# Kernel optimization log

Measured on AMD Instinct MI355X. Metric: run time of the kernel, lower is better.

Reference implementation:

```python
import jax, jax.numpy as jnp
import numpy as np

B, N, Q, Z, C, L = 1, 6, 20000, 4, 128, 4
IMG_H, IMG_W = 256, 704
PC_RANGE = (-50.0, -50.0, -4.0, 50.0, 50.0, 4.0)
NUM_FREQS = 10
EPS = 1e-5
LEVEL_HW = ((64, 176), (32, 88), (16, 44), (8, 22))


def _mlp(x, ws, bs):
    for i, (w, b) in enumerate(zip(ws, bs)):
        x = x @ w + b
        if i < len(ws) - 1:
            x = jax.nn.relu(x)
    return x


def _bilinear(feat_hwc, px, py):
    # feat_hwc: [H, W, C]; px, py: [P] pixel coords. align_corners=False, zero padding.
    H, W, _ = feat_hwc.shape
    x0 = jnp.floor(px).astype(jnp.int32)
    y0 = jnp.floor(py).astype(jnp.int32)
    wx = px - x0
    wy = py - y0

    def gather(yi, xi):
        inb = ((yi >= 0) & (yi < H) & (xi >= 0) & (xi < W)).astype(feat_hwc.dtype)
        return feat_hwc[jnp.clip(yi, 0, H - 1), jnp.clip(xi, 0, W - 1)] * inb[:, None]

    return (gather(y0, x0) * ((1 - wy) * (1 - wx))[:, None]
          + gather(y0, x0 + 1) * ((1 - wy) * wx)[:, None]
          + gather(y0 + 1, x0) * (wy * (1 - wx))[:, None]
          + gather(y0 + 1, x0 + 1) * (wy * wx)[:, None])


def _pointbev_forward(feats, reference_points, lidar2img,
                      pe_w1, pe_b1, pe_w2, pe_b2, wt_w, wt_b, hm_ws, hm_bs):
    pos = jnp.transpose(reference_points, (0, 2, 1, 3))            # [B,Q,Z,3] in [0,1]
    # sinusoidal positional encoding map (normalized=False: coords used as-is)
    freqs = (2.0 ** jnp.arange(NUM_FREQS, dtype=pos.dtype)) * jnp.pi
    ang = pos[..., None] * freqs                                   # [B,Q,Z,3,F]
    pe_in = jnp.concatenate([jnp.sin(ang), jnp.cos(ang)], axis=-1)
    pe_in = pe_in.reshape(pos.shape[:-1] + (3 * 2 * NUM_FREQS,))
    pos_emb = _mlp(pe_in, [pe_w1, pe_w2], [pe_b1, pe_b2])          # [B,Q,Z,C]
    scale_w = jax.nn.softmax(pos_emb @ wt_w + wt_b, axis=-1)       # [B,Q,Z,L]

    # unnormalize to metric lidar coords via pc_range
    lo = jnp.asarray(PC_RANGE[:3], pos.dtype)
    span = jnp.asarray(PC_RANGE[3:], pos.dtype) - lo
    pts4 = jnp.concatenate([pos * span + lo, jnp.ones_like(pos[..., :1])], axis=-1)
    cam = jnp.einsum('bnij,bqzj->bnqzi', lidar2img, pts4)          # [B,N,Q,Z,4]
    homo = cam[..., 2]
    uv = cam[..., :2] / jnp.maximum(homo, EPS)[..., None]
    u = uv[..., 0] / IMG_W
    v = uv[..., 1] / IMG_H
    valid = ((homo > EPS) & (u > 0.0) & (u < 1.0) & (v > 0.0) & (v < 1.0)).astype(pos.dtype)

    sampler = jax.vmap(_bilinear)
    uf = u.reshape(B * N, Q * Z)
    vf = v.reshape(B * N, Q * Z)
    out = jnp.zeros((B, Q, Z, C), pos.dtype)
    for l, feat in enumerate(feats):                               # L=4 fixed levels
        Hl, Wl = feat.shape[2], feat.shape[3]
        s = sampler(feat.reshape(B * N, Hl, Wl, C), uf * Wl - 0.5, vf * Hl - 0.5)
        s = s.reshape(B, N, Q, Z, C) * valid[..., None]            # mask invalid projections
        out = out + s.sum(axis=1) * scale_w[..., l, None]          # sum views, weight level
    out = (out + pos_emb).reshape(B, Q, Z * C)
    return _mlp(out, hm_ws, hm_bs)                                 # [B,Q,C]


def setup_inputs():
    key = jax.random.key(0)
    ks = jax.random.split(key, 32)
    inp = {}
    for l, (h, w) in enumerate(LEVEL_HW):
        inp[f"feat{l}"] = jax.random.normal(ks[l], (B, N, h, w, C), jnp.float32)
    inp["reference_points"] = jax.random.uniform(ks[8], (B, Z, Q, 3), jnp.float32)
    # structured nuScenes-like lidar2img = intrinsics @ extrinsics for a 6-camera ring
    l2i = np.zeros((B, N, 4, 4), np.float32)
    K = np.array([[400.0, 0.0, IMG_W / 2, 0.0],
                  [0.0, 400.0, IMG_H / 2, 0.0],
                  [0.0, 0.0, 1.0, 0.0],
                  [0.0, 0.0, 0.0, 1.0]], np.float32)
    for n in range(N):
        yaw = 2.0 * np.pi * n / N
        cy, sy = np.cos(yaw), np.sin(yaw)
        R = np.array([[-sy, cy, 0.0], [0.0, 0.0, -1.0], [cy, sy, 0.0]], np.float32)
        E = np.eye(4, dtype=np.float32)
        E[:3, :3] = R
        E[:3, 3] = [0.0, 1.5, 0.5]
        l2i[0, n] = K @ E
    inp["lidar2img"] = jnp.asarray(l2i)

    def lin(k, fi, fo):
        s = 1.0 / np.sqrt(fi)
        return jax.random.uniform(k, (fi, fo), jnp.float32, -s, s)

    d_in = 3 * 2 * NUM_FREQS
    inp["pe_w1"] = lin(ks[9], d_in, 2 * C); inp["pe_b1"] = jnp.zeros((2 * C,), jnp.float32)
    inp["pe_w2"] = lin(ks[10], 2 * C, C);   inp["pe_b2"] = jnp.zeros((C,), jnp.float32)
    inp["wt_w"] = lin(ks[11], C, L);        inp["wt_b"] = jnp.zeros((L,), jnp.float32)
    dims = [Z * C, 2 * Z * C, 2 * Z * C, 2 * Z * C, C]
    for i in range(4):
        inp[f"hm_w{i+1}"] = lin(ks[12 + i], dims[i], dims[i + 1])
        inp[f"hm_b{i+1}"] = jnp.zeros((dims[i + 1],), jnp.float32)
    return inp


def reference(feat0, feat1, feat2, feat3, reference_points, lidar2img,
              pe_w1, pe_b1, pe_w2, pe_b2, wt_w, wt_b,
              hm_w1, hm_b1, hm_w2, hm_b2, hm_w3, hm_b3, hm_w4, hm_b4):
    return _pointbev_forward((feat0, feat1, feat2, feat3), reference_points, lidar2img,
                             pe_w1, pe_b1, pe_w2, pe_b2, wt_w, wt_b,
                             [hm_w1, hm_w2, hm_w3, hm_w4], [hm_b1, hm_b2, hm_b3, hm_b4])
```

## Files before the change

### kernel.cpp

```cpp
#include <hip/hip_runtime.h>
#include <math.h>

#define QN 20000
#define PN 80000
#define CN 128
#define NVIEW 6

typedef __attribute__((ext_vector_type(8))) _Float16 h8;
typedef __attribute__((ext_vector_type(4))) _Float16 h4;
typedef __attribute__((ext_vector_type(4))) float f32x4;

__device__ __forceinline__ void gload16(const void* g, void* l) {
  __builtin_amdgcn_global_load_lds(
      (const __attribute__((address_space(1))) void*)g,
      (__attribute__((address_space(3))) void*)l, 16, 0, 0);
}

__global__ __launch_bounds__(256) void wtrans_all(
    const float* __restrict__ w0, const float* __restrict__ w1,
    const float* __restrict__ w2, const float* __restrict__ w3,
    const float* __restrict__ w4, const float* __restrict__ w5,
    _Float16* __restrict__ base) {
  __shared__ float t[32][33];
  int b = blockIdx.x;
  const float* W; _Float16* T; int K, N, Kp, nbx, lb;
  if (b < 16)        { W = w0; T = base + 0;       K = 60;   N = 256;  Kp = 64;   nbx = 8;  lb = b; }
  else if (b < 48)   { W = w1; T = base + 32768;   K = 256;  N = 128;  Kp = 256;  nbx = 4;  lb = b - 16; }
  else if (b < 560)  { W = w2; T = base + 98304;   K = 512;  N = 1024; Kp = 512;  nbx = 32; lb = b - 48; }
  else if (b < 1584) { W = w3; T = base + 1146880; K = 1024; N = 1024; Kp = 1024; nbx = 32; lb = b - 560; }
  else if (b < 2608) { W = w4; T = base + 3244032; K = 1024; N = 1024; Kp = 1024; nbx = 32; lb = b - 1584; }
  else               { W = w5; T = base + 5341184; K = 1024; N = 128;  Kp = 1024; nbx = 4;  lb = b - 2608; }
  const int n0 = (lb % nbx) * 32, k0 = (lb / nbx) * 32;
  const int tx = threadIdx.x & 31, ty = threadIdx.x >> 5;
  #pragma unroll
  for (int j = 0; j < 4; ++j) {
    int k = k0 + ty + j * 8;
    t[ty + j * 8][tx] = (k < K) ? W[(size_t)k * N + n0 + tx] : 0.f;
  }
  __syncthreads();
  #pragma unroll
  for (int j = 0; j < 4; ++j) {
    int n = n0 + ty + j * 8;
    int k = k0 + tx;
    T[(size_t)n * Kp + k] = (_Float16)t[tx][ty + j * 8];
  }
}

__global__ __launch_bounds__(256) void fcvt_kernel(
    const float* __restrict__ s0, const float* __restrict__ s1,
    const float* __restrict__ s2, const float* __restrict__ s3,
    _Float16* __restrict__ d) {
  size_t i = (size_t)blockIdx.x * 256 + threadIdx.x;
  if (i >= 2872320) return;
  const float* s; size_t off;
  if (i < 2162688)      { s = s0; off = 0; }
  else if (i < 2703360) { s = s1; off = 2162688; }
  else if (i < 2838528) { s = s2; off = 2703360; }
  else                  { s = s3; off = 2838528; }
  f32x4 v = *(const f32x4*)(s + (i - off) * 4);
  h4 o;
  o[0] = (_Float16)v[0]; o[1] = (_Float16)v[1];
  o[2] = (_Float16)v[2]; o[3] = (_Float16)v[3];
  *(h4*)(d + i * 4) = o;
}

__global__ __launch_bounds__(256) void pe_in_kernel(const float* __restrict__ rp,
                                                    _Float16* __restrict__ P) {
  int idx = blockIdx.x * 256 + threadIdx.x;
  if (idx >= PN * 64) return;
  int p = idx >> 6, k = idx & 63;
  float val = 0.f;
  if (k < 60) {
    int q = p >> 2, z = p & 3;
    int d = k / 20, r = k - d * 20;
    int j = (r >= 10) ? (r - 10) : r;
    float pos = rp[((size_t)z * QN + q) * 3 + d];
    float ang = pos * ((float)(1 << j) * 3.14159265358979323846f);
    val = (r >= 10) ? cosf(ang) : sinf(ang);
  }
  P[idx] = (_Float16)val;
}

template <bool RELU, int OUT>
__global__ __launch_bounds__(256, 4) void gemm_h(const _Float16* __restrict__ A,
                                                 const _Float16* __restrict__ B,
                                                 const float* __restrict__ bias,
                                                 float* __restrict__ Cf,
                                                 _Float16* __restrict__ Ch,
                                                 int M, int N, int K,
                                                 int nbn) {
  __shared__ _Float16 sm[2][2][4096];
  const int tid = threadIdx.x;
  const int wave = tid >> 6, lane = tid & 63;
  const int wr = wave >> 1, wc = wave & 1;
  const int g = lane >> 4, r16 = lane & 15;

  const int nwg = gridDim.x;
  const int q8 = nwg >> 3, r8 = nwg & 7;
  const int xcd = blockIdx.x & 7, sub = blockIdx.x >> 3;
  const int wg = (xcd < r8 ? xcd * (q8 + 1) : r8 * (q8 + 1) + (xcd - r8) * q8) + sub;
  const int bn = (wg % nbn) * 128;
  const int bm = (wg / nbn) * 128;
  const int nt = K >> 5;

  f32x4 acc[4][4];
  #pragma unroll
  for (int i = 0; i < 4; ++i)
    #pragma unroll
    for (int j = 0; j < 4; ++j) acc[i][j] = {0.f, 0.f, 0.f, 0.f};

  auto STAGE = [&](int buf, int t) {
    const int kof = t << 5;
    const int rsub = lane >> 2;
    const int slot0 = lane & 3;
    #pragma unroll
    for (int pl = 0; pl < 2; ++pl) {
      const _Float16* P = (pl == 0) ? A : B;
      const int rbase = (pl == 0) ? bm : bn;
      #pragma unroll
      for (int i = 0; i < 2; ++i) {
        int group = wave * 2 + i;
        int row = group * 16 + rsub;
        int slot = slot0 ^ ((row >> 1) & 3);
        int gr = rbase + row;
        if (pl == 0 && gr >= M) gr = M - 1;
        gload16(P + (size_t)gr * K + kof + slot * 8,
                &sm[buf][pl][group * 512]);
      }
    }
  };

  auto COMPUTE = [&](int buf) {
    h8 a[4], b[4];
    #pragma unroll
    for (int mi = 0; mi < 4; ++mi) {
      int row = wr * 64 + mi * 16 + r16;
      int off = row * 32 + ((g ^ ((row >> 1) & 3)) * 8);
      a[mi] = *(const h8*)&sm[buf][0][off];
    }
    #pragma unroll
    for (int ni = 0; ni < 4; ++ni) {
      int row = wc * 64 + ni * 16 + r16;
      int off = row * 32 + ((g ^ ((row >> 1) & 3)) * 8);
      b[ni] = *(const h8*)&sm[buf][1][off];
    }
    #pragma unroll
    for (int mi = 0; mi < 4; ++mi)
      #pragma unroll
      for (int ni = 0; ni < 4; ++ni)
        acc[mi][ni] = __builtin_amdgcn_mfma_f32_16x16x32_f16(a[mi], b[ni], acc[mi][ni], 0, 0, 0);
  };

  STAGE(0, 0);
  __syncthreads();

  for (int t = 0; t < nt; ++t) {
    if (t + 1 < nt) STAGE((t + 1) & 1, t + 1);
    COMPUTE(t & 1);
    __syncthreads();
  }

  #pragma unroll
  for (int mi = 0; mi < 4; ++mi) {
    int gr0 = bm + wr * 64 + mi * 16 + (lane >> 4) * 4;
    #pragma unroll
    for (int ni = 0; ni < 4; ++ni) {
      int gc = bn + wc * 64 + ni * 16 + r16;
      float bv = bias[gc];
      #pragma unroll
      for (int r = 0; r < 4; ++r) {
        int row = gr0 + r;
        if (row >= M) continue;
        float v = acc[mi][ni][r] + bv;
        if (RELU) v = fmaxf(v, 0.f);
        if (OUT == 0) Cf[(size_t)row * N + gc] = v;
        else          Ch[(size_t)row * N + gc] = (_Float16)v;
      }
    }
  }
}

__global__ __launch_bounds__(256) void sample_kernel(
    const _Float16* __restrict__ fbase,
    const float* __restrict__ rp, const float* __restrict__ l2i,
    const float* __restrict__ wtw, const float* __restrict__ wtb,
    const _Float16* __restrict__ posE, _Float16* __restrict__ X0) {
  __shared__ float sl2i[96];
  __shared__ float swtT[512];
  __shared__ float sb[4];
  const int tid = threadIdx.x;
  if (tid < 96) sl2i[tid] = l2i[tid];
  for (int i = tid; i < 512; i += 256) swtT[(i & 3) * 128 + (i >> 2)] = wtw[i];
  if (tid < 4) sb[tid] = wtb[tid];
  __syncthreads();

  const _Float16* FL[4] = {fbase, fbase + 8650752, fbase + 10813440,
                           fbase + 11354112};

  const int wave = tid >> 6, lane = tid & 63;
  const int half = lane >> 5, s = lane & 31;
  const int p = blockIdx.x * 8 + wave * 2 + half;
  const int q = p >> 2, z = p & 3;

  const float X  = rp[((size_t)z * QN + q) * 3 + 0] * 100.f - 50.f;
  const float Y  = rp[((size_t)z * QN + q) * 3 + 1] * 100.f - 50.f;
  const float Zc = rp[((size_t)z * QN + q) * 3 + 2] * 8.f - 4.f;

  const int c0 = s * 4;
  h4 pa = *(const h4*)(posE + (size_t)p * CN + c0);
  const float pe0 = (float)pa[0], pe1 = (float)pa[1];
  const float pe2 = (float)pa[2], pe3 = (float)pa[3];

  float l0 = pe0 * swtT[0 * 128 + c0] + pe1 * swtT[0 * 128 + c0 + 1]
           + pe2 * swtT[0 * 128 + c0 + 2] + pe3 * swtT[0 * 128 + c0 + 3];
  float l1 = pe0 * swtT[1 * 128 + c0] + pe1 * swtT[1 * 128 + c0 + 1]
           + pe2 * swtT[1 * 128 + c0 + 2] + pe3 * swtT[1 * 128 + c0 + 3];
  float l2 = pe0 * swtT[2 * 128 + c0] + pe1 * swtT[2 * 128 + c0 + 1]
           + pe2 * swtT[2 * 128 + c0 + 2] + pe3 * swtT[2 * 128 + c0 + 3];
  float l3 = pe0 * swtT[3 * 128 + c0] + pe1 * swtT[3 * 128 + c0 + 1]
           + pe2 * swtT[3 * 128 + c0 + 2] + pe3 * swtT[3 * 128 + c0 + 3];
  #pragma unroll
  for (int off = 16; off > 0; off >>= 1) {
    l0 += __shfl_xor(l0, off);
    l1 += __shfl_xor(l1, off);
    l2 += __shfl_xor(l2, off);
    l3 += __shfl_xor(l3, off);
  }
  l0 += sb[0]; l1 += sb[1]; l2 += sb[2]; l3 += sb[3];
  float mx = fmaxf(fmaxf(l0, l1), fmaxf(l2, l3));
  float ex0 = __expf(l0 - mx), ex1 = __expf(l1 - mx);
  float ex2 = __expf(l2 - mx), ex3 = __expf(l3 - mx);
  float esr = 1.f / (ex0 + ex1 + ex2 + ex3);
  float swl[4] = {ex0 * esr, ex1 * esr, ex2 * esr, ex3 * esr};

  float a0 = 0.f, a1 = 0.f, a2 = 0.f, a3 = 0.f;
  for (int n = 0; n < NVIEW; n++) {
    const float* Mx = sl2i + n * 16;
    float cam0 = Mx[0] * X + Mx[1] * Y + Mx[2]  * Zc + Mx[3];
    float cam1 = Mx[4] * X + Mx[5] * Y + Mx[6]  * Zc + Mx[7];
    float cam2 = Mx[8] * X + Mx[9] * Y + Mx[10] * Zc + Mx[11];
    float denom = fmaxf(cam2, 1e-5f);
    float u = cam0 / denom * (1.f / 704.f);
    float v = cam1 / denom * (1.f / 256.f);
    bool valid = (cam2 > 1e-5f) & (u > 0.f) & (u < 1.f) & (v > 0.f) & (v < 1.f);
    if (!valid) continue;
    float px3 = u * 22.f - 0.5f, py3 = v * 8.f - 0.5f;
    bool interior = (px3 >= 0.f) & (py3 >= 0.f) & (px3 < 21.f) & (py3 < 7.f);
    if (interior) {
      #pragma unroll
      for (int l = 0; l < 4; l++) {
        const int Hl = 64 >> l, Wl = 176 >> l;
        float pxl = u * (float)Wl - 0.5f;
        float pyl = v * (float)Hl - 0.5f;
        float fx = floorf(pxl), fy = floorf(pyl);
        int x0 = (int)fx, y0 = (int)fy;
        float wx = pxl - fx, wy = pyl - fy;
        float w1r = wy * swl[l], w0r = swl[l] - w1r;
        float w01 = w0r * wx, w00 = w0r - w01;
        float w11 = w1r * wx, w10 = w1r - w11;
        const _Float16* cp = FL[l]
            + ((size_t)n * (Hl * Wl) + (size_t)(y0 * Wl + x0)) * CN + c0;
        h4 v00 = *(const h4*)(cp);
        h4 v01 = *(const h4*)(cp + CN);
        h4 v10 = *(const h4*)(cp + Wl * CN);
        h4 v11 = *(const h4*)(cp + Wl * CN + CN);
        a0 = fmaf(w00, (float)v00[0], fmaf(w01, (float)v01[0], fmaf(w10, (float)v10[0], fmaf(w11, (float)v11[0], a0))));
        a1 = fmaf(w00, (float)v00[1], fmaf(w01, (float)v01[1], fmaf(w10, (float)v10[1], fmaf(w11, (float)v11[1], a1))));
        a2 = fmaf(w00, (float)v00[2], fmaf(w01, (float)v01[2], fmaf(w10, (float)v10[2], fmaf(w11, (float)v11[2], a2))));
        a3 = fmaf(w00, (float)v00[3], fmaf(w01, (float)v01[3], fmaf(w10, (float)v10[3], fmaf(w11, (float)v11[3], a3))));
      }
    } else {
      #pragma unroll
      for (int l = 0; l < 4; l++) {
        const int Hl = 64 >> l, Wl = 176 >> l;
        float pxl = u * (float)Wl - 0.5f;
        float pyl = v * (float)Hl - 0.5f;
        float fx = floorf(pxl), fy = floorf(pyl);
        int x0 = (int)fx, y0 = (int)fy;
        float wx = pxl - fx, wy = pyl - fy;
        float w1r = wy * swl[l], w0r = swl[l] - w1r;
        const float wxs[2] = {1.f - wx, wx};
        const float wrs[2] = {w0r, w1r};
        const _Float16* fb = FL[l] + (size_t)n * (Hl * Wl) * CN;
        #pragma unroll
        for (int cy = 0; cy < 2; cy++) {
          #pragma unroll
          for (int cx = 0; cx < 2; cx++) {
            int xi = x0 + cx, yi = y0 + cy;
            bool inb = ((unsigned)xi < (unsigned)Wl) & ((unsigned)yi < (unsigned)Hl);
            int off = inb ? (yi * Wl + xi) * CN : 0;
            float wgt = inb ? (wrs[cy] * wxs[cx]) : 0.f;
            h4 vv = *(const h4*)(fb + off + c0);
            a0 = fmaf(wgt, (float)vv[0], a0);
            a1 = fmaf(wgt, (float)vv[1], a1);
            a2 = fmaf(wgt, (float)vv[2], a2);
            a3 = fmaf(wgt, (float)vv[3], a3);
          }
        }
      }
    }
  }
  h4 o;
  o[0] = (_Float16)(a0 + pe0);
  o[1] = (_Float16)(a1 + pe1);
  o[2] = (_Float16)(a2 + pe2);
  o[3] = (_Float16)(a3 + pe3);
  *(h4*)&X0[(size_t)p * CN + c0] = o;
}

extern "C" void kernel_launch(void* const* d_in, const int* in_sizes, int n_in,
                              void* d_out, int out_size, void* d_ws, size_t ws_size,
                              hipStream_t stream) {
  const float* feat0 = (const float*)d_in[0];
  const float* feat1 = (const float*)d_in[1];
  const float* feat2 = (const float*)d_in[2];
  const float* feat3 = (const float*)d_in[3];
  const float* rp    = (const float*)d_in[4];
  const float* l2i   = (const float*)d_in[5];
  const float* pe_w1 = (const float*)d_in[6];
  const float* pe_b1 = (const float*)d_in[7];
  const float* pe_w2 = (const float*)d_in[8];
  const float* pe_b2 = (const float*)d_in[9];
  const float* wt_w  = (const float*)d_in[10];
  const float* wt_b  = (const float*)d_in[11];
  const float* hm_w1 = (const float*)d_in[12];
  const float* hm_b1 = (const float*)d_in[13];
  const float* hm_w2 = (const float*)d_in[14];
  const float* hm_b2 = (const float*)d_in[15];
  const float* hm_w3 = (const float*)d_in[16];
  const float* hm_b3 = (const float*)d_in[17];
  const float* hm_w4 = (const float*)d_in[18];
  const float* hm_b4 = (const float*)d_in[19];
  float* out = (float*)d_out;

  char* ws = (char*)d_ws;
  typedef _Float16 h16;
  h16* wPE1 = (h16*)(ws + 0);
  h16* wPE2 = (h16*)(ws + 65536);
  h16* wH1  = (h16*)(ws + 196608);
  h16* wH2  = (h16*)(ws + 2293760);
  h16* wH3  = (h16*)(ws + 6488064);
  h16* wH4  = (h16*)(ws + 10682368);

  h16* posE = (h16*)(ws + 11534336);
  h16* hpe  = (h16*)(ws + 53000192);
  h16* pein = (h16*)(ws + 94000128);
  h16* X0   = (h16*)(ws + 53000192);
  h16* H1   = (h16*)(ws + 94000128);
  h16* H2   = (h16*)(ws + 11534336);
  h16* H3   = (h16*)(ws + 94000128);
  h16* f16b = (h16*)(ws + 136000000);

  wtrans_all<<<2736, 256, 0, stream>>>(pe_w1, pe_w2, hm_w1, hm_w2, hm_w3, hm_w4,
                                       (h16*)ws);
  fcvt_kernel<<<(2872320 + 255) / 256, 256, 0, stream>>>(feat0, feat1, feat2,
                                                         feat3, f16b);

  pe_in_kernel<<<(PN * 64 + 255) / 256, 256, 0, stream>>>(rp, pein);

  gemm_h<true, 1><<<2 * 625, 256, 0, stream>>>(pein, wPE1, pe_b1, nullptr, hpe, PN, 256, 64, 2);
  gemm_h<false, 1><<<1 * 625, 256, 0, stream>>>(hpe, wPE2, pe_b2, nullptr, posE, PN, 128, 256, 1);

  sample_kernel<<<PN / 8, 256, 0, stream>>>(f16b, rp, l2i, wt_w, wt_b, posE, X0);

  gemm_h<true, 1><<<8 * 157, 256, 0, stream>>>(X0, wH1, hm_b1, nullptr, H1, QN, 1024, 512, 8);
  gemm_h<true, 1><<<8 * 157, 256, 0, stream>>>(H1, wH2, hm_b2, nullptr, H2, QN, 1024, 1024, 8);
  gemm_h<true, 1><<<8 * 157, 256, 0, stream>>>(H2, wH3, hm_b3, nullptr, H3, QN, 1024, 1024, 8);
  gemm_h<false, 0><<<1 * 157, 256, 0, stream>>>(H3, wH4, hm_b4, out, nullptr, QN, 128, 1024, 1);
}
```

Baseline: 320.2 us.

## Use smaller-tile GEMM for narrow layers and split softmax weights into own kernel

Adds a 64x128-tile GEMM variant with 128-thread blocks and uses it for the two N=128 layers (PE second layer and final head layer). This doubles the workgroup count so more CUs are busy. Separately, the scale-weight softmax moves out of sample_kernel into a dedicated lw_kernel that writes four floats per point to workspace. That trims per-thread work and shared memory in the gather kernel, at the cost of an extra launch and extra global traffic.

```diff
diff --git a/kernel.cpp b/kernel.cpp
--- a/kernel.cpp
+++ b/kernel.cpp
@@ -81,6 +81,50 @@
   P[idx] = (_Float16)val;
 }
 
+__global__ __launch_bounds__(256) void lw_kernel(const _Float16* __restrict__ posE,
+                                                 const float* __restrict__ wtw,
+                                                 const float* __restrict__ wtb,
+                                                 float* __restrict__ lw) {
+  __shared__ float swtT[512];
+  __shared__ float sb[4];
+  const int tid = threadIdx.x;
+  for (int i = tid; i < 512; i += 256) swtT[(i & 3) * 128 + (i >> 2)] = wtw[i];
+  if (tid < 4) sb[tid] = wtb[tid];
+  __syncthreads();
+
+  const int wave = tid >> 6, lane = tid & 63;
+  const int grp = lane >> 4, s = lane & 15;
+  const int p = blockIdx.x * 16 + wave * 4 + grp;
+  const int c0 = s * 8;
+  h8 pa = *(const h8*)(posE + (size_t)p * CN + c0);
+
+  float lg[4];
+  #pragma unroll
+  for (int l = 0; l < 4; ++l) {
+    const float* w = swtT + l * 128 + c0;
+    float acc = 0.f;
+    #pragma unroll
+    for (int j = 0; j < 8; ++j) acc = fmaf((float)pa[j], w[j], acc);
+    lg[l] = acc;
+  }
+  #pragma unroll
+  for (int off = 8; off > 0; off >>= 1) {
+    lg[0] += __shfl_xor(lg[0], off);
+    lg[1] += __shfl_xor(lg[1], off);
+    lg[2] += __shfl_xor(lg[2], off);
+    lg[3] += __shfl_xor(lg[3], off);
+  }
+  lg[0] += sb[0]; lg[1] += sb[1]; lg[2] += sb[2]; lg[3] += sb[3];
+  float mx = fmaxf(fmaxf(lg[0], lg[1]), fmaxf(lg[2], lg[3]));
+  float e0 = __expf(lg[0] - mx), e1 = __expf(lg[1] - mx);
+  float e2 = __expf(lg[2] - mx), e3 = __expf(lg[3] - mx);
+  float esr = 1.f / (e0 + e1 + e2 + e3);
+  if (s == 0) {
+    f32x4 o = {e0 * esr, e1 * esr, e2 * esr, e3 * esr};
+    *(f32x4*)(lw + (size_t)p * 4) = o;
+  }
+}
+
 template <bool RELU, int OUT>
 __global__ __launch_bounds__(256, 4) void gemm_h(const _Float16* __restrict__ A,
                                                  const _Float16* __restrict__ B,
@@ -180,18 +224,114 @@
   }
 }
 
+template <bool RELU, int OUT>
+__global__ __launch_bounds__(128, 3) void gemm_h64(const _Float16* __restrict__ A,
+                                                   const _Float16* __restrict__ B,
+                                                   const float* __restrict__ bias,
+                                                   float* __restrict__ Cf,
+                                                   _Float16* __restrict__ Ch,
+                                                   int M, int N, int K,
+                                                   int nbn) {
+  __shared__ _Float16 smA[2][64 * 32];
+  __shared__ _Float16 smB[2][128 * 32];
+  const int tid = threadIdx.x;
+  const int wave = tid >> 6, lane = tid & 63;
+  const int wc = wave;
+  const int g = lane >> 4, r16 = lane & 15;
+
+  const int nwg = gridDim.x;
+  const int q8 = nwg >> 3, r8 = nwg & 7;
+  const int xcd = blockIdx.x & 7, sub = blockIdx.x >> 3;
+  const int wg = (xcd < r8 ? xcd * (q8 + 1) : r8 * (q8 + 1) + (xcd - r8) * q8) + sub;
+  const int bn = (wg % nbn) * 128;
+  const int bm = (wg / nbn) * 64;
+  const int nt = K >> 5;
+
+  f32x4 acc[4][4];
+  #pragma unroll
+  for (int i = 0; i < 4; ++i)
+    #pragma unroll
+    for (int j = 0; j < 4; ++j) acc[i][j] = {0.f, 0.f, 0.f, 0.f};
+
+  auto STAGE = [&](int buf, int t) {
+    const int kof = t << 5;
+    const int rsub = lane >> 2;
+    const int slot0 = lane & 3;
+    #pragma unroll
+    for (int i = 0; i < 2; ++i) {
+      int group = wave * 2 + i;
+      int row = group * 16 + rsub;
+      int slot = slot0 ^ ((row >> 1) & 3);
+      int gr = bm + row; if (gr >= M) gr = M - 1;
+      gload16(A + (size_t)gr * K + kof + slot * 8, &smA[buf][group * 512]);
+    }
+    #pragma unroll
+    for (int i = 0; i < 4; ++i) {
+      int group = wave * 4 + i;
+      int row = group * 16 + rsub;
+      int slot = slot0 ^ ((row >> 1) & 3);
+      gload16(B + (size_t)(bn + row) * K + kof + slot * 8, &smB[buf][group * 512]);
+    }
+  };
+
+  auto COMPUTE = [&](int buf) {
+    h8 a[4], b[4];
+    #pragma unroll
+    for (int mi = 0; mi < 4; ++mi) {
+      int row = mi * 16 + r16;
+      int off = row * 32 + ((g ^ ((row >> 1) & 3)) * 8);
+      a[mi] = *(const h8*)&smA[buf][off];
+    }
+    #pragma unroll
+    for (int ni = 0; ni < 4; ++ni) {
+      int row = wc * 64 + ni * 16 + r16;
+      int off = row * 32 + ((g ^ ((row >> 1) & 3)) * 8);
+      b[ni] = *(const h8*)&smB[buf][off];
+    }
+    #pragma unroll
+    for (int mi = 0; mi < 4; ++mi)
+      #pragma unroll
+      for (int ni = 0; ni < 4; ++ni)
+        acc[mi][ni] = __builtin_amdgcn_mfma_f32_16x16x32_f16(a[mi], b[ni], acc[mi][ni], 0, 0, 0);
+  };
+
+  STAGE(0, 0);
+  __syncthreads();
+
+  for (int t = 0; t < nt; ++t) {
+    if (t + 1 < nt) STAGE((t + 1) & 1, t + 1);
+    COMPUTE(t & 1);
+    __syncthreads();
+  }
+
+  #pragma unroll
+  for (int mi = 0; mi < 4; ++mi) {
+    int gr0 = bm + mi * 16 + (lane >> 4) * 4;
+    #pragma unroll
+    for (int ni = 0; ni < 4; ++ni) {
+      int gc = bn + wc * 64 + ni * 16 + r16;
+      float bv = bias[gc];
+      #pragma unroll
+      for (int r = 0; r < 4; ++r) {
+        int row = gr0 + r;
+        if (row >= M) continue;
+        float v = acc[mi][ni][r] + bv;
+        if (RELU) v = fmaxf(v, 0.f);
+        if (OUT == 0) Cf[(size_t)row * N + gc] = v;
+        else          Ch[(size_t)row * N + gc] = (_Float16)v;
+      }
+    }
+  }
+}
+
 __global__ __launch_bounds__(256) void sample_kernel(
     const _Float16* __restrict__ fbase,
     const float* __restrict__ rp, const float* __restrict__ l2i,
-    const float* __restrict__ wtw, const float* __restrict__ wtb,
+    const float* __restrict__ lw,
     const _Float16* __restrict__ posE, _Float16* __restrict__ X0) {
   __shared__ float sl2i[96];
-  __shared__ float swtT[512];
-  __shared__ float sb[4];
   const int tid = threadIdx.x;
   if (tid < 96) sl2i[tid] = l2i[tid];
-  for (int i = tid; i < 512; i += 256) swtT[(i & 3) * 128 + (i >> 2)] = wtw[i];
-  if (tid < 4) sb[tid] = wtb[tid];
   __syncthreads();
 
   const _Float16* FL[4] = {fbase, fbase + 8650752, fbase + 10813440,
@@ -211,27 +351,8 @@
   const float pe0 = (float)pa[0], pe1 = (float)pa[1];
   const float pe2 = (float)pa[2], pe3 = (float)pa[3];
 
-  float l0 = pe0 * swtT[0 * 128 + c0] + pe1 * swtT[0 * 128 + c0 + 1]
-           + pe2 * swtT[0 * 128 + c0 + 2] + pe3 * swtT[0 * 128 + c0 + 3];
-  float l1 = pe0 * swtT[1 * 128 + c0] + pe1 * swtT[1 * 128 + c0 + 1]
-           + pe2 * swtT[1 * 128 + c0 + 2] + pe3 * swtT[1 * 128 + c0 + 3];
-  float l2 = pe0 * swtT[2 * 128 + c0] + pe1 * swtT[2 * 128 + c0 + 1]
-           + pe2 * swtT[2 * 128 + c0 + 2] + pe3 * swtT[2 * 128 + c0 + 3];
-  float l3 = pe0 * swtT[3 * 128 + c0] + pe1 * swtT[3 * 128 + c0 + 1]
-           + pe2 * swtT[3 * 128 + c0 + 2] + pe3 * swtT[3 * 128 + c0 + 3];
-  #pragma unroll
-  for (int off = 16; off > 0; off >>= 1) {
-    l0 += __shfl_xor(l0, off);
-    l1 += __shfl_xor(l1, off);
-    l2 += __shfl_xor(l2, off);
-    l3 += __shfl_xor(l3, off);
-  }
-  l0 += sb[0]; l1 += sb[1]; l2 += sb[2]; l3 += sb[3];
-  float mx = fmaxf(fmaxf(l0, l1), fmaxf(l2, l3));
-  float ex0 = __expf(l0 - mx), ex1 = __expf(l1 - mx);
-  float ex2 = __expf(l2 - mx), ex3 = __expf(l3 - mx);
-  float esr = 1.f / (ex0 + ex1 + ex2 + ex3);
-  float swl[4] = {ex0 * esr, ex1 * esr, ex2 * esr, ex3 * esr};
+  f32x4 lw4 = *(const f32x4*)(lw + (size_t)p * 4);
+  float swl[4] = {lw4[0], lw4[1], lw4[2], lw4[3]};
 
   float a0 = 0.f, a1 = 0.f, a2 = 0.f, a3 = 0.f;
   for (int n = 0; n < NVIEW; n++) {
@@ -342,14 +463,15 @@
   h16* wH3  = (h16*)(ws + 6488064);
   h16* wH4  = (h16*)(ws + 10682368);
 
-  h16* posE = (h16*)(ws + 11534336);
-  h16* hpe  = (h16*)(ws + 53000192);
-  h16* pein = (h16*)(ws + 94000128);
-  h16* X0   = (h16*)(ws + 53000192);
-  h16* H1   = (h16*)(ws + 94000128);
-  h16* H2   = (h16*)(ws + 11534336);
-  h16* H3   = (h16*)(ws + 94000128);
-  h16* f16b = (h16*)(ws + 136000000);
+  h16*   posE = (h16*)(ws + 11534336);
+  float* lwga = (float*)(ws + 33000000);
+  h16*   hpe  = (h16*)(ws + 53000192);
+  h16*   pein = (h16*)(ws + 94000128);
+  h16*   X0   = (h16*)(ws + 53000192);
+  h16*   H1   = (h16*)(ws + 94000128);
+  h16*   H2   = (h16*)(ws + 11534336);
+  h16*   H3   = (h16*)(ws + 94000128);
+  h16*   f16b = (h16*)(ws + 136000000);
 
   wtrans_all<<<2736, 256, 0, stream>>>(pe_w1, pe_w2, hm_w1, hm_w2, hm_w3, hm_w4,
                                        (h16*)ws);
@@ -359,12 +481,14 @@
   pe_in_kernel<<<(PN * 64 + 255) / 256, 256, 0, stream>>>(rp, pein);
 
   gemm_h<true, 1><<<2 * 625, 256, 0, stream>>>(pein, wPE1, pe_b1, nullptr, hpe, PN, 256, 64, 2);
-  gemm_h<false, 1><<<1 * 625, 256, 0, stream>>>(hpe, wPE2, pe_b2, nullptr, posE, PN, 128, 256, 1);
-
-  sample_kernel<<<PN / 8, 256, 0, stream>>>(f16b, rp, l2i, wt_w, wt_b, posE, X0);
+  gemm_h64<false, 1><<<1250, 128, 0, stream>>>(hpe, wPE2, pe_b2, nullptr, posE, PN, 128, 256, 1);
+
+  lw_kernel<<<PN / 16, 256, 0, stream>>>(posE, wt_w, wt_b, lwga);
+
+  sample_kernel<<<PN / 8, 256, 0, stream>>>(f16b, rp, l2i, lwga, posE, X0);
 
   gemm_h<true, 1><<<8 * 157, 256, 0, stream>>>(X0, wH1, hm_b1, nullptr, H1, QN, 1024, 512, 8);
   gemm_h<true, 1><<<8 * 157, 256, 0, stream>>>(H1, wH2, hm_b2, nullptr, H2, QN, 1024, 1024, 8);
   gemm_h<true, 1><<<8 * 157, 256, 0, stream>>>(H2, wH3, hm_b3, nullptr, H3, QN, 1024, 1024, 8);
-  gemm_h<false, 0><<<1 * 157, 256, 0, stream>>>(H3, wH4, hm_b4, out, nullptr, QN, 128, 1024, 1);
-}
+  gemm_h64<false, 0><<<313, 128, 0, stream>>>(H3, wH4, hm_b4, out, nullptr, QN, 128, 1024, 1);
+}
```

After: 322.6 us. Within noise of the previous version (+0.8%).

## Merge prep kernels into one launch and split softmax weights into own kernel

Applied to the files above, without the earlier changes.

Combines weight transpose, feature fp16 conversion and PE input generation into a single prep_all launch, cutting two kernel launches and their tails. Moves the per-point scale-weight logits and softmax out of sample_kernel into a separate lw_kernel that writes 4 floats per point, so sample_kernel only loads them. This adds one launch and an extra global round trip of the weights, in exchange for a lighter sample_kernel with less shared memory and fewer registers.

```diff
diff --git a/kernel.cpp b/kernel.cpp
--- a/kernel.cpp
+++ b/kernel.cpp
@@ -16,69 +16,109 @@
       (__attribute__((address_space(3))) void*)l, 16, 0, 0);
 }
 
-__global__ __launch_bounds__(256) void wtrans_all(
+__global__ __launch_bounds__(256) void prep_all(
     const float* __restrict__ w0, const float* __restrict__ w1,
     const float* __restrict__ w2, const float* __restrict__ w3,
     const float* __restrict__ w4, const float* __restrict__ w5,
-    _Float16* __restrict__ base) {
-  __shared__ float t[32][33];
-  int b = blockIdx.x;
-  const float* W; _Float16* T; int K, N, Kp, nbx, lb;
-  if (b < 16)        { W = w0; T = base + 0;       K = 60;   N = 256;  Kp = 64;   nbx = 8;  lb = b; }
-  else if (b < 48)   { W = w1; T = base + 32768;   K = 256;  N = 128;  Kp = 256;  nbx = 4;  lb = b - 16; }
-  else if (b < 560)  { W = w2; T = base + 98304;   K = 512;  N = 1024; Kp = 512;  nbx = 32; lb = b - 48; }
-  else if (b < 1584) { W = w3; T = base + 1146880; K = 1024; N = 1024; Kp = 1024; nbx = 32; lb = b - 560; }
-  else if (b < 2608) { W = w4; T = base + 3244032; K = 1024; N = 1024; Kp = 1024; nbx = 32; lb = b - 1584; }
-  else               { W = w5; T = base + 5341184; K = 1024; N = 128;  Kp = 1024; nbx = 4;  lb = b - 2608; }
-  const int n0 = (lb % nbx) * 32, k0 = (lb / nbx) * 32;
-  const int tx = threadIdx.x & 31, ty = threadIdx.x >> 5;
-  #pragma unroll
-  for (int j = 0; j < 4; ++j) {
-    int k = k0 + ty + j * 8;
-    t[ty + j * 8][tx] = (k < K) ? W[(size_t)k * N + n0 + tx] : 0.f;
-  }
-  __syncthreads();
-  #pragma unroll
-  for (int j = 0; j < 4; ++j) {
-    int n = n0 + ty + j * 8;
-    int k = k0 + tx;
-    T[(size_t)n * Kp + k] = (_Float16)t[tx][ty + j * 8];
-  }
-}
-
-__global__ __launch_bounds__(256) void fcvt_kernel(
+    _Float16* __restrict__ wbase,
     const float* __restrict__ s0, const float* __restrict__ s1,
     const float* __restrict__ s2, const float* __restrict__ s3,
-    _Float16* __restrict__ d) {
-  size_t i = (size_t)blockIdx.x * 256 + threadIdx.x;
-  if (i >= 2872320) return;
-  const float* s; size_t off;
-  if (i < 2162688)      { s = s0; off = 0; }
-  else if (i < 2703360) { s = s1; off = 2162688; }
-  else if (i < 2838528) { s = s2; off = 2703360; }
-  else                  { s = s3; off = 2838528; }
-  f32x4 v = *(const f32x4*)(s + (i - off) * 4);
-  h4 o;
-  o[0] = (_Float16)v[0]; o[1] = (_Float16)v[1];
-  o[2] = (_Float16)v[2]; o[3] = (_Float16)v[3];
-  *(h4*)(d + i * 4) = o;
-}
-
-__global__ __launch_bounds__(256) void pe_in_kernel(const float* __restrict__ rp,
-                                                    _Float16* __restrict__ P) {
-  int idx = blockIdx.x * 256 + threadIdx.x;
-  if (idx >= PN * 64) return;
-  int p = idx >> 6, k = idx & 63;
-  float val = 0.f;
-  if (k < 60) {
-    int q = p >> 2, z = p & 3;
-    int d = k / 20, r = k - d * 20;
-    int j = (r >= 10) ? (r - 10) : r;
-    float pos = rp[((size_t)z * QN + q) * 3 + d];
-    float ang = pos * ((float)(1 << j) * 3.14159265358979323846f);
-    val = (r >= 10) ? cosf(ang) : sinf(ang);
-  }
-  P[idx] = (_Float16)val;
+    _Float16* __restrict__ fdst,
+    const float* __restrict__ rp, _Float16* __restrict__ pedst) {
+  int b = blockIdx.x;
+  if (b < 2736) {
+    __shared__ float t[32][33];
+    const float* W; _Float16* T; int K, N, Kp, nbx, lb;
+    if (b < 16)        { W = w0; T = wbase + 0;       K = 60;   N = 256;  Kp = 64;   nbx = 8;  lb = b; }
+    else if (b < 48)   { W = w1; T = wbase + 32768;   K = 256;  N = 128;  Kp = 256;  nbx = 4;  lb = b - 16; }
+    else if (b < 560)  { W = w2; T = wbase + 98304;   K = 512;  N = 1024; Kp = 512;  nbx = 32; lb = b - 48; }
+    else if (b < 1584) { W = w3; T = wbase + 1146880; K = 1024; N = 1024; Kp = 1024; nbx = 32; lb = b - 560; }
+    else if (b < 2608) { W = w4; T = wbase + 3244032; K = 1024; N = 1024; Kp = 1024; nbx = 32; lb = b - 1584; }
+    else               { W = w5; T = wbase + 5341184; K = 1024; N = 128;  Kp = 1024; nbx = 4;  lb = b - 2608; }
+    const int n0 = (lb % nbx) * 32, k0 = (lb / nbx) * 32;
+    const int tx = threadIdx.x & 31, ty = threadIdx.x >> 5;
+    #pragma unroll
+    for (int j = 0; j < 4; ++j) {
+      int k = k0 + ty + j * 8;
+      t[ty + j * 8][tx] = (k < K) ? W[(size_t)k * N + n0 + tx] : 0.f;
+    }
+    __syncthreads();
+    #pragma unroll
+    for (int j = 0; j < 4; ++j) {
+      int n = n0 + ty + j * 8;
+      int k = k0 + tx;
+      T[(size_t)n * Kp + k] = (_Float16)t[tx][ty + j * 8];
+    }
+  } else if (b < 13956) {
+    size_t i = (size_t)(b - 2736) * 256 + threadIdx.x;
+    const float* s; size_t off;
+    if (i < 2162688)      { s = s0; off = 0; }
+    else if (i < 2703360) { s = s1; off = 2162688; }
+    else if (i < 2838528) { s = s2; off = 2703360; }
+    else                  { s = s3; off = 2838528; }
+    f32x4 v = *(const f32x4*)(s + (i - off) * 4);
+    h4 o;
+    o[0] = (_Float16)v[0]; o[1] = (_Float16)v[1];
+    o[2] = (_Float16)v[2]; o[3] = (_Float16)v[3];
+    *(h4*)(fdst + i * 4) = o;
+  } else {
+    int idx = (b - 13956) * 256 + threadIdx.x;
+    int p = idx >> 6, k = idx & 63;
+    float val = 0.f;
+    if (k < 60) {
+      int q = p >> 2, z = p & 3;
+      int d = k / 20, r = k - d * 20;
+      int j = (r >= 10) ? (r - 10) : r;
+      float pos = rp[((size_t)z * QN + q) * 3 + d];
+      float ang = pos * ((float)(1 << j) * 3.14159265358979323846f);
+      val = (r >= 10) ? cosf(ang) : sinf(ang);
+    }
+    pedst[idx] = (_Float16)val;
+  }
+}
+
+__global__ __launch_bounds__(256) void lw_kernel(const _Float16* __restrict__ posE,
+                                                 const float* __restrict__ wtw,
+                                                 const float* __restrict__ wtb,
+                                                 float* __restrict__ lw) {
+  __shared__ float swtT[512];
+  __shared__ float sb[4];
+  const int tid = threadIdx.x;
+  for (int i = tid; i < 512; i += 256) swtT[(i & 3) * 128 + (i >> 2)] = wtw[i];
+  if (tid < 4) sb[tid] = wtb[tid];
+  __syncthreads();
+
+  const int wave = tid >> 6, lane = tid & 63;
+  const int grp = lane >> 4, s = lane & 15;
+  const int p = blockIdx.x * 16 + wave * 4 + grp;
+  const int c0 = s * 8;
+  h8 pa = *(const h8*)(posE + (size_t)p * CN + c0);
+
+  float lg[4];
+  #pragma unroll
+  for (int l = 0; l < 4; ++l) {
+    const float* w = swtT + l * 128 + c0;
+    float acc = 0.f;
+    #pragma unroll
+    for (int j = 0; j < 8; ++j) acc = fmaf((float)pa[j], w[j], acc);
+    lg[l] = acc;
+  }
+  #pragma unroll
+  for (int off = 8; off > 0; off >>= 1) {
+    lg[0] += __shfl_xor(lg[0], off);
+    lg[1] += __shfl_xor(lg[1], off);
+    lg[2] += __shfl_xor(lg[2], off);
+    lg[3] += __shfl_xor(lg[3], off);
+  }
+  lg[0] += sb[0]; lg[1] += sb[1]; lg[2] += sb[2]; lg[3] += sb[3];
+  float mx = fmaxf(fmaxf(lg[0], lg[1]), fmaxf(lg[2], lg[3]));
+  float e0 = __expf(lg[0] - mx), e1 = __expf(lg[1] - mx);
+  float e2 = __expf(lg[2] - mx), e3 = __expf(lg[3] - mx);
+  float esr = 1.f / (e0 + e1 + e2 + e3);
+  if (s == 0) {
+    f32x4 o = {e0 * esr, e1 * esr, e2 * esr, e3 * esr};
+    *(f32x4*)(lw + (size_t)p * 4) = o;
+  }
 }
 
 template <bool RELU, int OUT>
@@ -183,15 +223,11 @@
 __global__ __launch_bounds__(256) void sample_kernel(
     const _Float16* __restrict__ fbase,
     const float* __restrict__ rp, const float* __restrict__ l2i,
-    const float* __restrict__ wtw, const float* __restrict__ wtb,
+    const float* __restrict__ lw,
     const _Float16* __restrict__ posE, _Float16* __restrict__ X0) {
   __shared__ float sl2i[96];
-  __shared__ float swtT[512];
-  __shared__ float sb[4];
   const int tid = threadIdx.x;
   if (tid < 96) sl2i[tid] = l2i[tid];
-  for (int i = tid; i < 512; i += 256) swtT[(i & 3) * 128 + (i >> 2)] = wtw[i];
-  if (tid < 4) sb[tid] = wtb[tid];
   __syncthreads();
 
   const _Float16* FL[4] = {fbase, fbase + 8650752, fbase + 10813440,
@@ -211,27 +247,8 @@
   const float pe0 = (float)pa[0], pe1 = (float)pa[1];
   const float pe2 = (float)pa[2], pe3 = (float)pa[3];
 
-  float l0 = pe0 * swtT[0 * 128 + c0] + pe1 * swtT[0 * 128 + c0 + 1]
-           + pe2 * swtT[0 * 128 + c0 + 2] + pe3 * swtT[0 * 128 + c0 + 3];
-  float l1 = pe0 * swtT[1 * 128 + c0] + pe1 * swtT[1 * 128 + c0 + 1]
-           + pe2 * swtT[1 * 128 + c0 + 2] + pe3 * swtT[1 * 128 + c0 + 3];
-  float l2 = pe0 * swtT[2 * 128 + c0] + pe1 * swtT[2 * 128 + c0 + 1]
-           + pe2 * swtT[2 * 128 + c0 + 2] + pe3 * swtT[2 * 128 + c0 + 3];
-  float l3 = pe0 * swtT[3 * 128 + c0] + pe1 * swtT[3 * 128 + c0 + 1]
-           + pe2 * swtT[3 * 128 + c0 + 2] + pe3 * swtT[3 * 128 + c0 + 3];
-  #pragma unroll
-  for (int off = 16; off > 0; off >>= 1) {
-    l0 += __shfl_xor(l0, off);
-    l1 += __shfl_xor(l1, off);
-    l2 += __shfl_xor(l2, off);
-    l3 += __shfl_xor(l3, off);
-  }
-  l0 += sb[0]; l1 += sb[1]; l2 += sb[2]; l3 += sb[3];
-  float mx = fmaxf(fmaxf(l0, l1), fmaxf(l2, l3));
-  float ex0 = __expf(l0 - mx), ex1 = __expf(l1 - mx);
-  float ex2 = __expf(l2 - mx), ex3 = __expf(l3 - mx);
-  float esr = 1.f / (ex0 + ex1 + ex2 + ex3);
-  float swl[4] = {ex0 * esr, ex1 * esr, ex2 * esr, ex3 * esr};
+  f32x4 lw4 = *(const f32x4*)(lw + (size_t)p * 4);
+  float swl[4] = {lw4[0], lw4[1], lw4[2], lw4[3]};
 
   float a0 = 0.f, a1 = 0.f, a2 = 0.f, a3 = 0.f;
   for (int n = 0; n < NVIEW; n++) {
@@ -342,26 +359,26 @@
   h16* wH3  = (h16*)(ws + 6488064);
   h16* wH4  = (h16*)(ws + 10682368);
 
-  h16* posE = (h16*)(ws + 11534336);
-  h16* hpe  = (h16*)(ws + 53000192);
-  h16* pein = (h16*)(ws + 94000128);
-  h16* X0   = (h16*)(ws + 53000192);
-  h16* H1   = (h16*)(ws + 94000128);
-  h16* H2   = (h16*)(ws + 11534336);
-  h16* H3   = (h16*)(ws + 94000128);
-  h16* f16b = (h16*)(ws + 136000000);
-
-  wtrans_all<<<2736, 256, 0, stream>>>(pe_w1, pe_w2, hm_w1, hm_w2, hm_w3, hm_w4,
-                                       (h16*)ws);
-  fcvt_kernel<<<(2872320 + 255) / 256, 256, 0, stream>>>(feat0, feat1, feat2,
-                                                         feat3, f16b);
-
-  pe_in_kernel<<<(PN * 64 + 255) / 256, 256, 0, stream>>>(rp, pein);
+  h16*   posE = (h16*)(ws + 11534336);
+  float* lwga = (float*)(ws + 33000000);
+  h16*   hpe  = (h16*)(ws + 53000192);
+  h16*   pein = (h16*)(ws + 94000128);
+  h16*   X0   = (h16*)(ws + 53000192);
+  h16*   H1   = (h16*)(ws + 94000128);
+  h16*   H2   = (h16*)(ws + 11534336);
+  h16*   H3   = (h16*)(ws + 94000128);
+  h16*   f16b = (h16*)(ws + 136000000);
+
+  prep_all<<<33956, 256, 0, stream>>>(pe_w1, pe_w2, hm_w1, hm_w2, hm_w3, hm_w4,
+                                      (h16*)ws, feat0, feat1, feat2, feat3,
+                                      f16b, rp, pein);
 
   gemm_h<true, 1><<<2 * 625, 256, 0, stream>>>(pein, wPE1, pe_b1, nullptr, hpe, PN, 256, 64, 2);
   gemm_h<false, 1><<<1 * 625, 256, 0, stream>>>(hpe, wPE2, pe_b2, nullptr, posE, PN, 128, 256, 1);
 
-  sample_kernel<<<PN / 8, 256, 0, stream>>>(f16b, rp, l2i, wt_w, wt_b, posE, X0);
+  lw_kernel<<<PN / 16, 256, 0, stream>>>(posE, wt_w, wt_b, lwga);
+
+  sample_kernel<<<PN / 8, 256, 0, stream>>>(f16b, rp, l2i, lwga, posE, X0);
 
   gemm_h<true, 1><<<8 * 157, 256, 0, stream>>>(X0, wH1, hm_b1, nullptr, H1, QN, 1024, 512, 8);
   gemm_h<true, 1><<<8 * 157, 256, 0, stream>>>(H1, wH2, hm_b2, nullptr, H2, QN, 1024, 1024, 8);
```

New measurement: 314.3 us. Within noise of the previous version (-1.8%).
